# Kernel optimization log

Measured on AMD Instinct MI355X. Metric: run time of the kernel, lower is better.

Reference implementation:

```python
import jax, jax.numpy as jnp
import numpy as np

Nq, Ns, D, H, S, B, MS, MB = 30000, 400, 128, 128, 200, 256, 4, 4
P = H + 3 * D  # pred_in_feature = 512


def _lin(k, out_f, in_f):
    sc = 1.0 / np.sqrt(in_f)
    return sc * jax.random.normal(k, (out_f, in_f), jnp.float32)


def setup_inputs() -> dict:
    key = jax.random.key(0)
    ks = jax.random.split(key, 40)
    inp = {}
    inp['q_emb'] = 0.1 * jax.random.normal(ks[0], (Nq, D), jnp.float32)
    inp['s_emb'] = 0.1 * jax.random.normal(ks[1], (Ns, D), jnp.float32)
    inp['ans_emb'] = jax.random.normal(ks[2], (4, D), jnp.float32)
    inp['label_emb'] = jax.random.normal(ks[3], (2, D), jnp.float32)
    inp['gru_Wi'] = _lin(ks[4], 3 * H, 5 * D)
    inp['gru_Wh'] = _lin(ks[5], 3 * H, H)
    inp['gru_bi'] = jnp.zeros((3 * H,), jnp.float32)
    inp['gru_bh'] = jnp.zeros((3 * H,), jnp.float32)
    for i, nm in enumerate(['s2s', 's2q', 'q2q', 'q2s']):
        inp[nm + '_W'] = _lin(ks[6 + i], D, D)
        inp[nm + '_b'] = jnp.zeros((D,), jnp.float32)
    inp['l1_W'] = _lin(ks[10], P, P); inp['l1_b'] = jnp.zeros((P,), jnp.float32)
    inp['l2_W'] = _lin(ks[11], P, P); inp['l2_b'] = jnp.zeros((P,), jnp.float32)
    inp['out_W'] = _lin(ks[12], 1, P); inp['out_b'] = jnp.zeros((1,), jnp.float32)
    inp['test_mask'] = jnp.ones((S, B), jnp.float32)
    inp['valid_mask'] = jnp.ones((S, B), jnp.float32)
    inp['local_test_mask'] = jnp.ones((S, B), jnp.float32)
    inp['subject_mask'] = jnp.ones((S, B, MB), jnp.float32)
    inp['q_mask'] = jnp.ones((Nq, MS), jnp.float32)
    inp['labels'] = jnp.round(jax.random.uniform(ks[13], (S, B), jnp.float32))
    inp['ans'] = jax.random.randint(ks[14], (S, B), 0, 4, jnp.int32)
    inp['correct_ans'] = jax.random.randint(ks[15], (S, B), 0, 4, jnp.int32)
    inp['subject_ids'] = jax.random.randint(ks[16], (S, B, MB), 0, Ns, jnp.int32)
    inp['q_ids'] = jax.random.randint(ks[17], (S, B), 0, Nq, jnp.int32)
    q_map = jax.random.randint(ks[18], (Nq, MS), 0, Ns, jnp.int32)
    inp['q_map'] = q_map
    inp['edge_q'] = jnp.repeat(jnp.arange(Nq, dtype=jnp.int32), MS)  # [Nq*MS]
    inp['edge_s'] = q_map.reshape(-1)  # subject segment id per edge
    return inp


def reference(q_emb, s_emb, ans_emb, label_emb, gru_Wi, gru_Wh, gru_bi, gru_bh,
              s2s_W, s2s_b, s2q_W, s2q_b, q2q_W, q2q_b, q2s_W, q2s_b,
              l1_W, l1_b, l2_W, l2_b, out_W, out_b,
              test_mask, valid_mask, local_test_mask, subject_mask, q_mask, labels,
              ans, correct_ans, subject_ids, q_ids, q_map, edge_q, edge_s):
    n_subject = s_emb.shape[0]
    # --- GCN layer 1: question -> subject aggregation (fused segment mean) ---
    q2s_proj = q_emb @ q2s_W.T + q2s_b                      # [Nq, D]
    sums = jax.ops.segment_sum(q2s_proj[edge_q], edge_s, num_segments=n_subject)
    cnts = jax.ops.segment_sum(jnp.ones_like(edge_s, q_emb.dtype), edge_s,
                               num_segments=n_subject)       # [Ns]
    nq_s = sums / jnp.maximum(cnts, 1.0)[:, None]            # mean over neighbor questions
    sq_s = s_emb @ s2s_W.T + s2s_b
    subjects_1 = jnp.where(cnts[:, None] > 0, jnp.tanh(nq_s + sq_s), 0.0)  # [Ns, D]
    # --- GCN layer 2: subject -> question aggregation ---
    nq = jnp.sum(subjects_1[q_map] * q_mask[..., None], axis=1) / \
         jnp.sum(q_mask, axis=-1, keepdims=True)             # [Nq, D]
    questions_1 = jnp.tanh(nq @ s2q_W.T + s2q_b + q_emb @ q2q_W.T + q2q_b)
    # --- sequence features ---
    mask = (test_mask * valid_mask * local_test_mask)[..., None]  # [S,B,1]
    subjects = jnp.sum(subjects_1[subject_ids] * subject_mask[..., None], axis=2)  # [S,B,D]
    questions = questions_1[q_ids]                            # [S,B,D]
    ans_embed = ans_emb[ans] * mask
    correct_ans_embed = ans_emb[correct_ans]
    label_embed = label_emb[labels.astype(jnp.int32)] * mask
    lstm_input = jnp.concatenate(
        [ans_embed, correct_ans_embed, label_embed, questions, subjects], axis=-1)  # [S,B,5D]
    # --- GRU (PyTorch gate layout: r|z|n), dropout=0 / eval mode ---
    xp = lstm_input @ gru_Wi.T + gru_bi                      # [S,B,3H]
    hdim = gru_Wh.shape[1]
    h0 = jnp.zeros((lstm_input.shape[1], hdim), lstm_input.dtype)

    def step(h, xp_t):
        gh = h @ gru_Wh.T + gru_bh
        xr, xz, xn = jnp.split(xp_t, 3, axis=-1)
        hr, hz, hn = jnp.split(gh, 3, axis=-1)
        r = jax.nn.sigmoid(xr + hr)
        z = jax.nn.sigmoid(xz + hz)
        n = jnp.tanh(xn + r * hn)
        h_new = (1.0 - z) * n + z * h
        return h_new, h_new

    _, outs = jax.lax.scan(step, h0, xp)                     # [S,B,H]
    forward_ht = jnp.concatenate([h0[None], outs[:-1]], axis=0)  # shifted hidden states
    # --- prediction head with residual ---
    pred_input = jnp.concatenate(
        [questions, subjects, forward_ht, correct_ans_embed], axis=-1)  # [S,B,P]
    h1 = jax.nn.relu(pred_input @ l1_W.T + l1_b)
    h2 = jax.nn.relu(h1 @ l2_W.T + l2_b)
    logits = ((h2 + pred_input) @ out_W.T + out_b)[..., 0]   # [S,B]
    # BCEWithLogits: softplus(x) - x*y
    per_elem = jax.nn.softplus(logits) - logits * labels
    mask2d = mask[..., 0]
    loss = jnp.mean(per_elem * mask2d) / jnp.mean(mask2d)
    probs = jax.nn.sigmoid(logits)
    return loss, probs
```

## Files before the change

### kernel.cpp

```cpp
#include <hip/hip_runtime.h>
#include <hip/hip_bf16.h>
#include <math.h>

#define NQ 30000
#define NS 400
#define DD 128
#define HH 128
#define SS 200
#define BB 256
#define MSq 4
#define MBs 4
#define PP 512
#define SB (SS*BB)
#define G3 384
#define QPB 16
#define REPL 8
#define GBLK 32
#define TST3 (GBLK*3*1024)

typedef __hip_bfloat16 bf16;
typedef __attribute__((ext_vector_type(8))) short bf16x8;
typedef __attribute__((ext_vector_type(4))) float f32x4;
typedef __attribute__((ext_vector_type(4))) _Float16 f16x4;

__device__ __forceinline__ float sigf(float x){ return 1.0f/(1.0f+expf(-x)); }
__device__ __forceinline__ float sigf2(float x){ return 1.0f/(1.0f+__expf(-x)); }
__device__ __forceinline__ float tanhf2(float x){ return 1.0f - 2.0f/(__expf(2.0f*x)+1.0f); }
__device__ __forceinline__ float bfu2f(unsigned short u){
  unsigned int x = ((unsigned int)u)<<16;
  return __uint_as_float(x);
}

__global__ __launch_bounds__(128) void tables_k(const float* __restrict__ ans_emb,
        const float* __restrict__ label_emb, const float* __restrict__ Wi,
        float* __restrict__ Tans, float* __restrict__ Tcae, float* __restrict__ Tlab){
  int j = blockIdx.x*128 + threadIdx.x;
  if (j >= G3) return;
  const float* wr = Wi + (size_t)j*640;
  for (int a=0;a<4;a++){
    float acc=0.f;
    for (int k=0;k<DD;k++) acc += ans_emb[a*DD+k]*wr[k];
    Tans[a*G3+j]=acc;
  }
  for (int a=0;a<4;a++){
    float acc=0.f;
    for (int k=0;k<DD;k++) acc += ans_emb[a*DD+k]*wr[128+k];
    Tcae[a*G3+j]=acc;
  }
  for (int l=0;l<2;l++){
    float acc=0.f;
    for (int k=0;k<DD;k++) acc += label_emb[l*DD+k]*wr[256+k];
    Tlab[l*G3+j]=acc;
  }
}

__global__ __launch_bounds__(256) void conv_w_k(const float* __restrict__ l1W,
        const float* __restrict__ l2W, const float* __restrict__ Wi,
        bf16* __restrict__ l1Wb, bf16* __restrict__ l2Wb, bf16* __restrict__ WiB){
  int i = blockIdx.x*256 + threadIdx.x;
  if (i < 512*512){
    l1Wb[i] = __float2bfloat16(l1W[i]);
    l2Wb[i] = __float2bfloat16(l2W[i]);
  }
  if (i < 384*256){
    int j = i >> 8, k = i & 255;
    WiB[i] = __float2bfloat16(Wi[j*640 + 384 + k]);
  }
}

__global__ __launch_bounds__(128) void q2s_scatter(const float* __restrict__ q_emb,
        const float* __restrict__ W, const float* __restrict__ bias,
        const int* __restrict__ q_map, float* __restrict__ sums, float* __restrict__ cnts){
  __shared__ float qe[QPB][DD];
  int q0 = blockIdx.x*QPB;
  int tid = threadIdx.x;
  float* S = sums + (size_t)(blockIdx.x & (REPL-1))*51200;
  float* C = cnts + (size_t)(blockIdx.x & (REPL-1))*400;
  for (int r=0;r<QPB;r++) qe[r][tid] = q_emb[(size_t)(q0+r)*DD + tid];
  __syncthreads();
  float acc[QPB];
  #pragma unroll
  for (int r=0;r<QPB;r++) acc[r] = bias[tid];
  const float4* wr = (const float4*)(W + (size_t)tid*DD);
  #pragma unroll 4
  for (int k4=0;k4<DD/4;k4++){
    float4 w = wr[k4];
    #pragma unroll
    for (int r=0;r<QPB;r++){
      acc[r] += w.x*qe[r][k4*4] + w.y*qe[r][k4*4+1] + w.z*qe[r][k4*4+2] + w.w*qe[r][k4*4+3];
    }
  }
  for (int r=0;r<QPB;r++){
    int q = q0+r;
    #pragma unroll
    for (int m=0;m<MSq;m++){
      int s = q_map[q*MSq+m];
      atomicAdd(&S[(size_t)s*DD + tid], acc[r]);
      if (tid==0) atomicAdd(&C[s], 1.0f);
    }
  }
}

__global__ __launch_bounds__(128) void subjects1_k(const float* __restrict__ s_emb,
        const float* __restrict__ W, const float* __restrict__ bias,
        const float* __restrict__ sums, const float* __restrict__ cnts,
        float* __restrict__ out){
  __shared__ float se[DD];
  int s = blockIdx.x; int tid = threadIdx.x;
  se[tid] = s_emb[(size_t)s*DD+tid];
  __syncthreads();
  float acc = bias[tid];
  const float4* wr = (const float4*)(W + (size_t)tid*DD);
  for (int k4=0;k4<DD/4;k4++){
    float4 w = wr[k4];
    acc += w.x*se[k4*4] + w.y*se[k4*4+1] + w.z*se[k4*4+2] + w.w*se[k4*4+3];
  }
  float c = 0.f, sm = 0.f;
  #pragma unroll
  for (int r=0;r<REPL;r++){
    c  += cnts[r*400 + s];
    sm += sums[(size_t)r*51200 + (size_t)s*DD + tid];
  }
  float v = 0.f;
  if (c > 0.f) v = tanhf(sm/fmaxf(c,1.f) + acc);
  out[(size_t)s*DD+tid] = v;
}

__global__ __launch_bounds__(128) void questions1_k(const float* __restrict__ q_emb,
        const float* __restrict__ subj1, const int* __restrict__ q_map,
        const float* __restrict__ q_mask,
        const float* __restrict__ s2qW, const float* __restrict__ s2qb,
        const float* __restrict__ q2qW, const float* __restrict__ q2qb,
        bf16* __restrict__ q1out){
  __shared__ float qe[QPB][DD];
  __shared__ float nq[QPB][DD];
  int q0 = blockIdx.x*QPB; int tid = threadIdx.x;
  for (int r=0;r<QPB;r++){
    int q = q0+r;
    qe[r][tid] = q_emb[(size_t)q*DD+tid];
    float sum=0.f, wsum=0.f;
    #pragma unroll
    for (int m=0;m<MSq;m++){
      float w = q_mask[q*MSq+m];
      sum += subj1[(size_t)q_map[q*MSq+m]*DD + tid]*w;
      wsum += w;
    }
    nq[r][tid] = sum / wsum;
  }
  __syncthreads();
  float acc[QPB];
  #pragma unroll
  for (int r=0;r<QPB;r++) acc[r] = s2qb[tid]+q2qb[tid];
  const float4* w1 = (const float4*)(s2qW + (size_t)tid*DD);
  const float4* w2 = (const float4*)(q2qW + (size_t)tid*DD);
  #pragma unroll 2
  for (int k4=0;k4<DD/4;k4++){
    float4 a = w1[k4]; float4 b = w2[k4];
    #pragma unroll
    for (int r=0;r<QPB;r++){
      acc[r] += a.x*nq[r][k4*4] + a.y*nq[r][k4*4+1] + a.z*nq[r][k4*4+2] + a.w*nq[r][k4*4+3]
              + b.x*qe[r][k4*4] + b.y*qe[r][k4*4+1] + b.z*qe[r][k4*4+2] + b.w*qe[r][k4*4+3];
    }
  }
  for (int r=0;r<QPB;r++) q1out[(size_t)(q0+r)*DD+tid] = __float2bfloat16(tanhf(acc[r]));
}

__global__ __launch_bounds__(128) void assemble_k(const bf16* __restrict__ q1,
        const float* __restrict__ subj1, const float* __restrict__ ans_emb,
        const int* __restrict__ cans, const int* __restrict__ sub_ids,
        const float* __restrict__ sub_mask, const int* __restrict__ q_ids,
        bf16* __restrict__ pred){
  int i = blockIdx.x; int d = threadIdx.x;
  size_t base = (size_t)i*PP;
  pred[base + d] = q1[(size_t)q_ids[i]*DD + d];
  float s = 0.f;
  #pragma unroll
  for (int m=0;m<MBs;m++)
    s += subj1[(size_t)sub_ids[i*MBs+m]*DD+d]*sub_mask[i*MBs+m];
  pred[base+128+d] = __float2bfloat16(s);
  pred[base+384+d] = __float2bfloat16(ans_emb[(size_t)cans[i]*DD + d]);
}

__global__ __launch_bounds__(256) void gemm_xp(const bf16* __restrict__ pred,
        const bf16* __restrict__ WiB, const float* __restrict__ bi,
        const float* __restrict__ bh,
        const float* __restrict__ Tans, const float* __restrict__ Tcae,
        const float* __restrict__ Tlab,
        const float* __restrict__ tm, const float* __restrict__ vm,
        const float* __restrict__ lm,
        const int* __restrict__ ans, const int* __restrict__ cans,
        const float* __restrict__ labels, _Float16* __restrict__ xp3){
  int lane = threadIdx.x & 63; int wid = threadIdx.x >> 6;
  int wy = wid >> 1, wx = wid & 1;
  int mbase = blockIdx.x*128 + wy*64;
  int lr = lane & 15, kg = (lane >> 4) * 8;
  for (int ny=0; ny<3; ny++){
    int nbase = ny*128 + wx*64;
    f32x4 acc[4][4];
    #pragma unroll
    for (int i=0;i<4;i++)
      #pragma unroll
      for (int j=0;j<4;j++) acc[i][j] = (f32x4){0.f,0.f,0.f,0.f};
    for (int k=0; k<256; k+=32){
      bf16x8 af[4], bfr[4];
      #pragma unroll
      for (int mi=0;mi<4;mi++)
        af[mi] = *(const bf16x8*)(pred + (size_t)(mbase+mi*16+lr)*PP + k + kg);
      #pragma unroll
      for (int ni=0;ni<4;ni++)
        bfr[ni] = *(const bf16x8*)(WiB + (size_t)(nbase+ni*16+lr)*256 + k + kg);
      #pragma unroll
      for (int mi=0;mi<4;mi++)
        #pragma unroll
        for (int ni=0;ni<4;ni++)
          acc[mi][ni] = __builtin_amdgcn_mfma_f32_16x16x32_bf16(af[mi], bfr[ni], acc[mi][ni], 0, 0, 0);
    }
    #pragma unroll
    for (int mi=0;mi<4;mi++){
      #pragma unroll
      for (int r=0;r<4;r++){
        int row = mbase + mi*16 + (lane>>4)*4 + r;
        int t = row >> 8, b = row & 255;
        size_t base = (((size_t)t*GBLK + (b>>3))*3)*1024 + (b&7);
        float mk = tm[row]*vm[row]*lm[row];
        int a = ans[row], ca = cans[row], lb = (int)labels[row];
        #pragma unroll
        for (int ni=0;ni<4;ni++){
          int c = nbase + ni*16 + lr;
          int g = c >> 7, dd = c & 127;
          float v = acc[mi][ni][r] + bi[c]
              + mk*Tans[a*G3+c] + Tcae[ca*G3+c] + mk*Tlab[lb*G3+c];
          if (g < 2) v += bh[c];
          xp3[base + (size_t)(g*1024 + dd*8)] = (_Float16)v;
        }
      }
    }
  }
}

__global__ __launch_bounds__(512, 1) void gemm_l1l2(const bf16* __restrict__ pred,
        const bf16* __restrict__ W1, const float* __restrict__ b1,
        const bf16* __restrict__ W2, const float* __restrict__ b2,
        const float* __restrict__ outW, float* __restrict__ logits){
  __shared__ __align__(16) char hl[64*1024];
  const int lane = threadIdx.x & 63;
  const int wx = threadIdx.x >> 6;
  const int nbase = wx*64;
  const int mbase = blockIdx.x*64;
  const int lr = lane & 15, lg = lane >> 4, kg = lg*8;

  {
    f32x4 acc[4][4];
    #pragma unroll
    for (int i=0;i<4;i++)
      #pragma unroll
      for (int j=0;j<4;j++) acc[i][j] = (f32x4){0.f,0.f,0.f,0.f};
    float pres[4] = {0.f,0.f,0.f,0.f};
    for (int k=0; k<512; k+=32){
      bf16x8 af[4], bfr[4];
      #pragma unroll
      for (int mi=0;mi<4;mi++)
        af[mi] = *(const bf16x8*)(pred + (size_t)(mbase+mi*16+lr)*PP + k + kg);
      #pragma unroll
      for (int ni=0;ni<4;ni++)
        bfr[ni] = *(const bf16x8*)(W1 + (size_t)(nbase+ni*16+lr)*PP + k + kg);
      #pragma unroll
      for (int mi=0;mi<4;mi++)
        #pragma unroll
        for (int ni=0;ni<4;ni++)
          acc[mi][ni] = __builtin_amdgcn_mfma_f32_16x16x32_bf16(af[mi], bfr[ni], acc[mi][ni], 0, 0, 0);
      if (wx == 0){
        float4 o0 = *(const float4*)(outW + k + kg);
        float4 o1 = *(const float4*)(outW + k + kg + 4);
        #pragma unroll
        for (int mi=0;mi<4;mi++){
          const unsigned short* au = (const unsigned short*)&af[mi];
          pres[mi] += bfu2f(au[0])*o0.x + bfu2f(au[1])*o0.y + bfu2f(au[2])*o0.z + bfu2f(au[3])*o0.w
                    + bfu2f(au[4])*o1.x + bfu2f(au[5])*o1.y + bfu2f(au[6])*o1.z + bfu2f(au[7])*o1.w;
        }
      }
    }
    #pragma unroll
    for (int mi=0;mi<4;mi++){
      #pragma unroll
      for (int ni=0;ni<4;ni++){
        int c = nbase + ni*16 + lr;
        float bia = b1[c];
        #pragma unroll
        for (int r=0;r<4;r++){
          int rw = mi*16 + lg*4 + r;
          int addr = (rw*1024 + c*2) ^ ((rw&7)<<4);
          *(bf16*)(hl + addr) = __float2bfloat16(fmaxf(acc[mi][ni][r] + bia, 0.f));
        }
      }
    }
    if (wx == 0){
      #pragma unroll
      for (int mi=0;mi<4;mi++){
        float v = pres[mi];
        v += __shfl_xor(v, 16);
        v += __shfl_xor(v, 32);
        if (lg == 0) atomicAdd(&logits[mbase + mi*16 + lr], v);
      }
    }
  }
  __syncthreads();
  {
    f32x4 acc[4][4];
    #pragma unroll
    for (int i=0;i<4;i++)
      #pragma unroll
      for (int j=0;j<4;j++) acc[i][j] = (f32x4){0.f,0.f,0.f,0.f};
    for (int k=0; k<512; k+=32){
      bf16x8 af[4], bfr[4];
      #pragma unroll
      for (int mi=0;mi<4;mi++){
        int rw = mi*16 + lr;
        int addr = (rw*1024 + (k+kg)*2) ^ ((rw&7)<<4);
        af[mi] = *(const bf16x8*)(hl + addr);
      }
      #pragma unroll
      for (int ni=0;ni<4;ni++)
        bfr[ni] = *(const bf16x8*)(W2 + (size_t)(nbase+ni*16+lr)*PP + k + kg);
      #pragma unroll
      for (int mi=0;mi<4;mi++)
        #pragma unroll
        for (int ni=0;ni<4;ni++)
          acc[mi][ni] = __builtin_amdgcn_mfma_f32_16x16x32_bf16(af[mi], bfr[ni], acc[mi][ni], 0, 0, 0);
    }
    #pragma unroll
    for (int mi=0;mi<4;mi++){
      #pragma unroll
      for (int r=0;r<4;r++){
        int row = mbase + mi*16 + lg*4 + r;
        float p = 0.f;
        #pragma unroll
        for (int ni=0;ni<4;ni++){
          int c = nbase + ni*16 + lr;
          p += fmaxf(acc[mi][ni][r] + b2[c], 0.f) * outW[c];
        }
        p += __shfl_xor(p,1);
        p += __shfl_xor(p,2);
        p += __shfl_xor(p,4);
        p += __shfl_xor(p,8);
        if (lr == 0) atomicAdd(&logits[row], p);
      }
    }
  }
}

__global__ __launch_bounds__(512, 1) void gru_scan_mfma(const _Float16* __restrict__ xp3,
        const float* __restrict__ Wh, const float* __restrict__ bh,
        bf16* __restrict__ pred){
  __shared__ __align__(16) char hbf[8192];
  const int tid  = threadIdx.x;
  const int lane = tid & 63;
  const int w    = tid >> 6;
  const int lr   = lane & 15;
  const int lg   = lane >> 4;
  const int d    = w*16 + lr;
  const int bg0  = blockIdx.x * 8;

  union U8 { bf16x8 v; unsigned short s[8]; };
  bf16x8 wf0[4], wf1[4], wf2[4];
  #pragma unroll
  for (int kk=0; kk<4; kk++){
    #pragma unroll
    for (int g=0; g<3; g++){
      const float* src = Wh + (size_t)(g*HH + d)*HH + kk*32 + lg*8;
      U8 u;
      #pragma unroll
      for (int j=0;j<8;j++){
        bf16 bv = __float2bfloat16(src[j]);
        u.s[j] = reinterpret_cast<unsigned short&>(bv);
      }
      if (g==0) wf0[kk]=u.v; else if (g==1) wf1[kk]=u.v; else wf2[kk]=u.v;
    }
  }
  const float bh2 = bh[2*HH+d];

  int rdaddr[4];
  #pragma unroll
  for (int kk=0;kk<4;kk++) rdaddr[kk] = lr*256 + ((kk*64 + lg*16) ^ ((lr&7)<<4));
  int wraddr[4];
  #pragma unroll
  for (int q=0;q<4;q++){
    int B_ = lg*4 + q;
    wraddr[q] = B_*256 + ((2*d) ^ ((B_&7)<<4));
  }
  const int fB = tid >> 4, fblk = tid & 15;
  const int faddr = fB*256 + ((fblk*16) ^ ((fB&7)<<4));
  bf16* fptr = pred + ((size_t)bg0 + fB)*PP + 256 + fblk*8;
  const size_t PSTRIDE = (size_t)BB*PP;

  float h0=0.f, h1v=0.f, h2v=0.f, h3v=0.f;
  ((unsigned long long*)hbf)[tid]       = 0ULL;
  ((unsigned long long*)hbf)[tid + 512] = 0ULL;

  const char* xb = (const char*)(xp3 + (size_t)blockIdx.x*3*1024 + d*8 + (lg&1)*4);

#define GSET(s) \
  f16x4 x##s##r = *(const f16x4*)(xb + (size_t)(s)*TST3*2); \
  f16x4 x##s##z = *(const f16x4*)(xb + (size_t)(s)*TST3*2 + 2048); \
  f16x4 x##s##n = *(const f16x4*)(xb + (size_t)(s)*TST3*2 + 4096);
  GSET(0) GSET(1) GSET(2) GSET(3) GSET(4) GSET(5) GSET(6) GSET(7)
#undef GSET

  __syncthreads();

#define GATEQ(Q, CR, CZ, CN, HV) { \
    float r  = sigf2((float)(CR) + ac0[Q]); \
    float zg = sigf2((float)(CZ) + ac1[Q]); \
    float n  = tanhf2((float)(CN) + r*(ac2[Q] + bh2)); \
    HV = (1.f - zg)*n + zg*HV; }

#define GSTEP(s, RO_, WO_) { \
    f32x4 ac0 = (f32x4){0.f,0.f,0.f,0.f}, ac1 = ac0, ac2 = ac0; \
    _Pragma("unroll") for (int kk=0; kk<4; kk++){ \
      bf16x8 a = *(const bf16x8*)(hbf + (RO_) + rdaddr[kk]); \
      ac0 = __builtin_amdgcn_mfma_f32_16x16x32_bf16(a, wf0[kk], ac0, 0,0,0); \
      ac1 = __builtin_amdgcn_mfma_f32_16x16x32_bf16(a, wf1[kk], ac1, 0,0,0); \
      ac2 = __builtin_amdgcn_mfma_f32_16x16x32_bf16(a, wf2[kk], ac2, 0,0,0); \
    } \
    if (tid < 128){   \
      int4 hv = *(const int4*)(hbf + (RO_) + faddr); \
      *(int4*)fptr = hv; \
    } \
    fptr += PSTRIDE; \
    GATEQ(0, x##s##r.x, x##s##z.x, x##s##n.x, h0) \
    GATEQ(1, x##s##r.y, x##s##z.y, x##s##n.y, h1v) \
    GATEQ(2, x##s##r.z, x##s##z.z, x##s##n.z, h2v) \
    GATEQ(3, x##s##r.w, x##s##z.w, x##s##n.w, h3v) \
    if (lg < 2){ \
      *(bf16*)(hbf + (WO_) + wraddr[0]) = __float2bfloat16(h0); \
      *(bf16*)(hbf + (WO_) + wraddr[1]) = __float2bfloat16(h1v); \
      *(bf16*)(hbf + (WO_) + wraddr[2]) = __float2bfloat16(h2v); \
      *(bf16*)(hbf + (WO_) + wraddr[3]) = __float2bfloat16(h3v); \
    } \
    x##s##r = *(const f16x4*)(xb + (size_t)((s)+8)*TST3*2); \
    x##s##z = *(const f16x4*)(xb + (size_t)((s)+8)*TST3*2 + 2048); \
    x##s##n = *(const f16x4*)(xb + (size_t)((s)+8)*TST3*2 + 4096); \
    asm volatile("s_waitcnt lgkmcnt(0)" ::: "memory"); \
    __builtin_amdgcn_s_barrier(); \
    __builtin_amdgcn_sched_barrier(0); \
  }

  for (int it=0; it<SS/8; ++it){
    GSTEP(0, 0,    4096)
    GSTEP(1, 4096, 0)
    GSTEP(2, 0,    4096)
    GSTEP(3, 4096, 0)
    GSTEP(4, 0,    4096)
    GSTEP(5, 4096, 0)
    GSTEP(6, 0,    4096)
    GSTEP(7, 4096, 0)
    xb += (size_t)8*TST3*2;
  }
#undef GSTEP
#undef GATEQ
}

__global__ __launch_bounds__(256) void loss_probs_k(const float* __restrict__ logits,
        const float* __restrict__ labels, const float* __restrict__ tm,
        const float* __restrict__ vm, const float* __restrict__ lm,
        const float* __restrict__ out_b, float* __restrict__ out,
        float* __restrict__ lacc){
  int i = blockIdx.x*256 + threadIdx.x;
  float x = logits[i] + out_b[0];
  float lb = labels[i];
  float mk = tm[i]*vm[i]*lm[i];
  float sp = fmaxf(x,0.f) + log1pf(expf(-fabsf(x)));
  float pe = (sp - x*lb)*mk;
  out[1+i] = sigf(x);
  float v0 = pe, v1 = mk;
  for (int o=32;o>0;o>>=1){ v0 += __shfl_down(v0,o); v1 += __shfl_down(v1,o); }
  if ((threadIdx.x & 63)==0){ atomicAdd(&lacc[0], v0); atomicAdd(&lacc[1], v1); }
}

__global__ void finalize_k(const float* __restrict__ lacc, float* __restrict__ out){
  out[0] = lacc[0]/lacc[1];
}

extern "C" void kernel_launch(void* const* d_in, const int* in_sizes, int n_in,
                              void* d_out, int out_size, void* d_ws, size_t ws_size,
                              hipStream_t stream) {
  const float* q_emb   = (const float*)d_in[0];
  const float* s_emb   = (const float*)d_in[1];
  const float* ans_emb = (const float*)d_in[2];
  const float* lab_emb = (const float*)d_in[3];
  const float* gru_Wi  = (const float*)d_in[4];
  const float* gru_Wh  = (const float*)d_in[5];
  const float* gru_bi  = (const float*)d_in[6];
  const float* gru_bh  = (const float*)d_in[7];
  const float* s2s_W   = (const float*)d_in[8];
  const float* s2s_b   = (const float*)d_in[9];
  const float* s2q_W   = (const float*)d_in[10];
  const float* s2q_b   = (const float*)d_in[11];
  const float* q2q_W   = (const float*)d_in[12];
  const float* q2q_b   = (const float*)d_in[13];
  const float* q2s_W   = (const float*)d_in[14];
  const float* q2s_b   = (const float*)d_in[15];
  const float* l1_W    = (const float*)d_in[16];
  const float* l1_b    = (const float*)d_in[17];
  const float* l2_W    = (const float*)d_in[18];
  const float* l2_b    = (const float*)d_in[19];
  const float* out_W   = (const float*)d_in[20];
  const float* out_b   = (const float*)d_in[21];
  const float* tm      = (const float*)d_in[22];
  const float* vm      = (const float*)d_in[23];
  const float* lm      = (const float*)d_in[24];
  const float* smask   = (const float*)d_in[25];
  const float* q_mask  = (const float*)d_in[26];
  const float* labels  = (const float*)d_in[27];
  const int*   ans     = (const int*)d_in[28];
  const int*   cans    = (const int*)d_in[29];
  const int*   sub_ids = (const int*)d_in[30];
  const int*   q_ids   = (const int*)d_in[31];
  const int*   q_map   = (const int*)d_in[32];

  char* wsb = (char*)d_ws;
  size_t off = 0;
  auto alloc = [&](size_t bytes) -> char* {
    char* p = wsb + off;
    off += (bytes + 255) & ~(size_t)255;
    return p;
  };
  float* sums   = (float*)alloc((size_t)REPL*51200*4);
  float* cnts   = (float*)alloc((size_t)REPL*400*4);
  float* subj1  = (float*)alloc(51200*4);
  float* Tans   = (float*)alloc(4*G3*4);
  float* Tcae   = (float*)alloc(4*G3*4);
  float* Tlab   = (float*)alloc(2*G3*4);
  float* lacc   = (float*)alloc(2*4);
  float* logits = (float*)alloc((size_t)SB*4);
  bf16*  l1Wb   = (bf16*) alloc((size_t)512*512*2);
  bf16*  l2Wb   = (bf16*) alloc((size_t)512*512*2);
  bf16*  WiB    = (bf16*) alloc((size_t)384*256*2);
  bf16*  q1     = (bf16*) alloc((size_t)NQ*DD*2);
  bf16*  pred   = (bf16*) alloc((size_t)SB*PP*2);
  _Float16* xp3 = (_Float16*)alloc(((size_t)SS+8)*TST3*2);
  float* out    = (float*)d_out;

  hipMemsetAsync(sums, 0, (size_t)REPL*(51200+400)*sizeof(float), stream);
  hipMemsetAsync(lacc, 0, 2*sizeof(float), stream);
  hipMemsetAsync(logits, 0, (size_t)SB*sizeof(float), stream);

  tables_k<<<dim3(3), dim3(128), 0, stream>>>(ans_emb, lab_emb, gru_Wi, Tans, Tcae, Tlab);
  conv_w_k<<<dim3(1024), dim3(256), 0, stream>>>(l1_W, l2_W, gru_Wi, l1Wb, l2Wb, WiB);
  q2s_scatter<<<dim3(NQ/QPB), dim3(128), 0, stream>>>(q_emb, q2s_W, q2s_b, q_map, sums, cnts);
  subjects1_k<<<dim3(NS), dim3(128), 0, stream>>>(s_emb, s2s_W, s2s_b, sums, cnts, subj1);
  questions1_k<<<dim3(NQ/QPB), dim3(128), 0, stream>>>(q_emb, subj1, q_map, q_mask,
                                                       s2q_W, s2q_b, q2q_W, q2q_b, q1);
  assemble_k<<<dim3(SB), dim3(128), 0, stream>>>(q1, subj1, ans_emb, cans, sub_ids, smask, q_ids, pred);
  gemm_xp<<<dim3(400), dim3(256), 0, stream>>>(pred, WiB, gru_bi, gru_bh, Tans, Tcae, Tlab,
                                               tm, vm, lm, ans, cans, labels, xp3);
  gru_scan_mfma<<<dim3(GBLK), dim3(512), 0, stream>>>(xp3, gru_Wh, gru_bh, pred);
  gemm_l1l2<<<dim3(SB/64), dim3(512), 0, stream>>>(pred, l1Wb, l1_b, l2Wb, l2_b, out_W, logits);
  loss_probs_k<<<dim3(SB/256), dim3(256), 0, stream>>>(logits, labels, tm, vm, lm, out_b, out, lacc);
  finalize_k<<<dim3(1), dim3(1), 0, stream>>>(lacc, out);
}
```

Measured before the change: 922.8 us.

## Retune scatter replication, grid-stride assemble, split xp GEMM grid, shallower GRU prefetch

```diff
diff --git a/kernel.cpp b/kernel.cpp
--- a/kernel.cpp
+++ b/kernel.cpp
@@ -14,7 +14,7 @@
 #define SB (SS*BB)
 #define G3 384
 #define QPB 16
-#define REPL 8
+#define REPL 64
 #define GBLK 32
 #define TST3 (GBLK*3*1024)
 
@@ -24,8 +24,12 @@
 typedef __attribute__((ext_vector_type(4))) _Float16 f16x4;
 
 __device__ __forceinline__ float sigf(float x){ return 1.0f/(1.0f+expf(-x)); }
-__device__ __forceinline__ float sigf2(float x){ return 1.0f/(1.0f+__expf(-x)); }
-__device__ __forceinline__ float tanhf2(float x){ return 1.0f - 2.0f/(__expf(2.0f*x)+1.0f); }
+__device__ __forceinline__ float sigr(float x){
+  return __builtin_amdgcn_rcpf(1.0f + __expf(-x));
+}
+__device__ __forceinline__ float tanhr(float x){
+  return 1.0f - 2.0f*__builtin_amdgcn_rcpf(__expf(2.0f*x) + 1.0f);
+}
 __device__ __forceinline__ float bfu2f(unsigned short u){
   unsigned int x = ((unsigned int)u)<<16;
   return __uint_as_float(x);
@@ -116,7 +120,6 @@
     acc += w.x*se[k4*4] + w.y*se[k4*4+1] + w.z*se[k4*4+2] + w.w*se[k4*4+3];
   }
   float c = 0.f, sm = 0.f;
-  #pragma unroll
   for (int r=0;r<REPL;r++){
     c  += cnts[r*400 + s];
     sm += sums[(size_t)r*51200 + (size_t)s*DD + tid];
@@ -165,20 +168,23 @@
   for (int r=0;r<QPB;r++) q1out[(size_t)(q0+r)*DD+tid] = __float2bfloat16(tanhf(acc[r]));
 }
 
-__global__ __launch_bounds__(128) void assemble_k(const bf16* __restrict__ q1,
+__global__ __launch_bounds__(256) void assemble_k(const bf16* __restrict__ q1,
         const float* __restrict__ subj1, const float* __restrict__ ans_emb,
         const int* __restrict__ cans, const int* __restrict__ sub_ids,
         const float* __restrict__ sub_mask, const int* __restrict__ q_ids,
         bf16* __restrict__ pred){
-  int i = blockIdx.x; int d = threadIdx.x;
-  size_t base = (size_t)i*PP;
-  pred[base + d] = q1[(size_t)q_ids[i]*DD + d];
-  float s = 0.f;
-  #pragma unroll
-  for (int m=0;m<MBs;m++)
-    s += subj1[(size_t)sub_ids[i*MBs+m]*DD+d]*sub_mask[i*MBs+m];
-  pred[base+128+d] = __float2bfloat16(s);
-  pred[base+384+d] = __float2bfloat16(ans_emb[(size_t)cans[i]*DD + d]);
+  const int total = SB*DD;
+  for (int idx = blockIdx.x*256 + threadIdx.x; idx < total; idx += 1024*256){
+    int i = idx >> 7, d = idx & 127;
+    size_t base = (size_t)i*PP;
+    pred[base + d] = q1[(size_t)q_ids[i]*DD + d];
+    float s = 0.f;
+    #pragma unroll
+    for (int m=0;m<MBs;m++)
+      s += subj1[(size_t)sub_ids[i*MBs+m]*DD+d]*sub_mask[i*MBs+m];
+    pred[base+128+d] = __float2bfloat16(s);
+    pred[base+384+d] = __float2bfloat16(ans_emb[(size_t)cans[i]*DD + d]);
+  }
 }
 
 __global__ __launch_bounds__(256) void gemm_xp(const bf16* __restrict__ pred,
@@ -193,46 +199,44 @@
   int lane = threadIdx.x & 63; int wid = threadIdx.x >> 6;
   int wy = wid >> 1, wx = wid & 1;
   int mbase = blockIdx.x*128 + wy*64;
+  int nbase = blockIdx.y*128 + wx*64;
   int lr = lane & 15, kg = (lane >> 4) * 8;
-  for (int ny=0; ny<3; ny++){
-    int nbase = ny*128 + wx*64;
-    f32x4 acc[4][4];
-    #pragma unroll
-    for (int i=0;i<4;i++)
-      #pragma unroll
-      for (int j=0;j<4;j++) acc[i][j] = (f32x4){0.f,0.f,0.f,0.f};
-    for (int k=0; k<256; k+=32){
-      bf16x8 af[4], bfr[4];
-      #pragma unroll
-      for (int mi=0;mi<4;mi++)
-        af[mi] = *(const bf16x8*)(pred + (size_t)(mbase+mi*16+lr)*PP + k + kg);
+  f32x4 acc[4][4];
+  #pragma unroll
+  for (int i=0;i<4;i++)
+    #pragma unroll
+    for (int j=0;j<4;j++) acc[i][j] = (f32x4){0.f,0.f,0.f,0.f};
+  for (int k=0; k<256; k+=32){
+    bf16x8 af[4], bfr[4];
+    #pragma unroll
+    for (int mi=0;mi<4;mi++)
+      af[mi] = *(const bf16x8*)(pred + (size_t)(mbase+mi*16+lr)*PP + k + kg);
+    #pragma unroll
+    for (int ni=0;ni<4;ni++)
+      bfr[ni] = *(const bf16x8*)(WiB + (size_t)(nbase+ni*16+lr)*256 + k + kg);
+    #pragma unroll
+    for (int mi=0;mi<4;mi++)
       #pragma unroll
       for (int ni=0;ni<4;ni++)
-        bfr[ni] = *(const bf16x8*)(WiB + (size_t)(nbase+ni*16+lr)*256 + k + kg);
-      #pragma unroll
-      for (int mi=0;mi<4;mi++)
-        #pragma unroll
-        for (int ni=0;ni<4;ni++)
-          acc[mi][ni] = __builtin_amdgcn_mfma_f32_16x16x32_bf16(af[mi], bfr[ni], acc[mi][ni], 0, 0, 0);
-    }
-    #pragma unroll
-    for (int mi=0;mi<4;mi++){
-      #pragma unroll
-      for (int r=0;r<4;r++){
-        int row = mbase + mi*16 + (lane>>4)*4 + r;
-        int t = row >> 8, b = row & 255;
-        size_t base = (((size_t)t*GBLK + (b>>3))*3)*1024 + (b&7);
-        float mk = tm[row]*vm[row]*lm[row];
-        int a = ans[row], ca = cans[row], lb = (int)labels[row];
-        #pragma unroll
-        for (int ni=0;ni<4;ni++){
-          int c = nbase + ni*16 + lr;
-          int g = c >> 7, dd = c & 127;
-          float v = acc[mi][ni][r] + bi[c]
-              + mk*Tans[a*G3+c] + Tcae[ca*G3+c] + mk*Tlab[lb*G3+c];
-          if (g < 2) v += bh[c];
-          xp3[base + (size_t)(g*1024 + dd*8)] = (_Float16)v;
-        }
+        acc[mi][ni] = __builtin_amdgcn_mfma_f32_16x16x32_bf16(af[mi], bfr[ni], acc[mi][ni], 0, 0, 0);
+  }
+  #pragma unroll
+  for (int mi=0;mi<4;mi++){
+    #pragma unroll
+    for (int r=0;r<4;r++){
+      int row = mbase + mi*16 + (lane>>4)*4 + r;
+      int t = row >> 8, b = row & 255;
+      size_t base = (((size_t)t*GBLK + (b>>3))*3)*1024 + (b&7);
+      float mk = tm[row]*vm[row]*lm[row];
+      int a = ans[row], ca = cans[row], lb = (int)labels[row];
+      #pragma unroll
+      for (int ni=0;ni<4;ni++){
+        int c = nbase + ni*16 + lr;
+        int g = c >> 7, dd = c & 127;
+        float v = acc[mi][ni][r] + bi[c]
+            + mk*Tans[a*G3+c] + Tcae[ca*G3+c] + mk*Tlab[lb*G3+c];
+        if (g < 2) v += bh[c];
+        xp3[base + (size_t)(g*1024 + dd*8)] = (_Float16)v;
       }
     }
   }
@@ -248,7 +252,6 @@
   const int nbase = wx*64;
   const int mbase = blockIdx.x*64;
   const int lr = lane & 15, lg = lane >> 4, kg = lg*8;
-
   {
     f32x4 acc[4][4];
     #pragma unroll
@@ -398,23 +401,23 @@
   ((unsigned long long*)hbf)[tid + 512] = 0ULL;
 
   const char* xb = (const char*)(xp3 + (size_t)blockIdx.x*3*1024 + d*8 + (lg&1)*4);
-
-#define GSET(s) \
-  f16x4 x##s##r = *(const f16x4*)(xb + (size_t)(s)*TST3*2); \
-  f16x4 x##s##z = *(const f16x4*)(xb + (size_t)(s)*TST3*2 + 2048); \
-  f16x4 x##s##n = *(const f16x4*)(xb + (size_t)(s)*TST3*2 + 4096);
-  GSET(0) GSET(1) GSET(2) GSET(3) GSET(4) GSET(5) GSET(6) GSET(7)
-#undef GSET
+  f16x4 xrA = *(const f16x4*)(xb);
+  f16x4 xzA = *(const f16x4*)(xb + 2048);
+  f16x4 xnA = *(const f16x4*)(xb + 4096);
+  f16x4 xrB = *(const f16x4*)(xb + (size_t)TST3*2);
+  f16x4 xzB = *(const f16x4*)(xb + (size_t)TST3*2 + 2048);
+  f16x4 xnB = *(const f16x4*)(xb + (size_t)TST3*2 + 4096);
+  const char* xt = xb + 2*(size_t)TST3*2;
 
   __syncthreads();
 
 #define GATEQ(Q, CR, CZ, CN, HV) { \
-    float r  = sigf2((float)(CR) + ac0[Q]); \
-    float zg = sigf2((float)(CZ) + ac1[Q]); \
-    float n  = tanhf2((float)(CN) + r*(ac2[Q] + bh2)); \
+    float r  = sigr((float)(CR) + ac0[Q]); \
+    float zg = sigr((float)(CZ) + ac1[Q]); \
+    float n  = tanhr((float)(CN) + r*(ac2[Q] + bh2)); \
     HV = (1.f - zg)*n + zg*HV; }
 
-#define GSTEP(s, RO_, WO_) { \
+#define GSTEP(RO_, WO_, XR, XZ, XN) { \
     f32x4 ac0 = (f32x4){0.f,0.f,0.f,0.f}, ac1 = ac0, ac2 = ac0; \
     _Pragma("unroll") for (int kk=0; kk<4; kk++){ \
       bf16x8 a = *(const bf16x8*)(hbf + (RO_) + rdaddr[kk]); \
@@ -422,39 +425,33 @@
       ac1 = __builtin_amdgcn_mfma_f32_16x16x32_bf16(a, wf1[kk], ac1, 0,0,0); \
       ac2 = __builtin_amdgcn_mfma_f32_16x16x32_bf16(a, wf2[kk], ac2, 0,0,0); \
     } \
-    if (tid < 128){   \
+    if (tid < 128){ \
       int4 hv = *(const int4*)(hbf + (RO_) + faddr); \
       *(int4*)fptr = hv; \
     } \
     fptr += PSTRIDE; \
-    GATEQ(0, x##s##r.x, x##s##z.x, x##s##n.x, h0) \
-    GATEQ(1, x##s##r.y, x##s##z.y, x##s##n.y, h1v) \
-    GATEQ(2, x##s##r.z, x##s##z.z, x##s##n.z, h2v) \
-    GATEQ(3, x##s##r.w, x##s##z.w, x##s##n.w, h3v) \
+    GATEQ(0, (XR).x, (XZ).x, (XN).x, h0) \
+    GATEQ(1, (XR).y, (XZ).y, (XN).y, h1v) \
+    GATEQ(2, (XR).z, (XZ).z, (XN).z, h2v) \
+    GATEQ(3, (XR).w, (XZ).w, (XN).w, h3v) \
     if (lg < 2){ \
       *(bf16*)(hbf + (WO_) + wraddr[0]) = __float2bfloat16(h0); \
       *(bf16*)(hbf + (WO_) + wraddr[1]) = __float2bfloat16(h1v); \
       *(bf16*)(hbf + (WO_) + wraddr[2]) = __float2bfloat16(h2v); \
       *(bf16*)(hbf + (WO_) + wraddr[3]) = __float2bfloat16(h3v); \
     } \
-    x##s##r = *(const f16x4*)(xb + (size_t)((s)+8)*TST3*2); \
-    x##s##z = *(const f16x4*)(xb + (size_t)((s)+8)*TST3*2 + 2048); \
-    x##s##n = *(const f16x4*)(xb + (size_t)((s)+8)*TST3*2 + 4096); \
+    XR = *(const f16x4*)(xt); \
+    XZ = *(const f16x4*)(xt + 2048); \
+    XN = *(const f16x4*)(xt + 4096); \
+    xt += (size_t)TST3*2; \
     asm volatile("s_waitcnt lgkmcnt(0)" ::: "memory"); \
     __builtin_amdgcn_s_barrier(); \
     __builtin_amdgcn_sched_barrier(0); \
   }
 
-  for (int it=0; it<SS/8; ++it){
-    GSTEP(0, 0,    4096)
-    GSTEP(1, 4096, 0)
-    GSTEP(2, 0,    4096)
-    GSTEP(3, 4096, 0)
-    GSTEP(4, 0,    4096)
-    GSTEP(5, 4096, 0)
-    GSTEP(6, 0,    4096)
-    GSTEP(7, 4096, 0)
-    xb += (size_t)8*TST3*2;
+  for (int t=0; t<SS; t+=2){
+    GSTEP(0,    4096, xrA, xzA, xnA)
+    GSTEP(4096, 0,    xrB, xzB, xnB)
   }
 #undef GSTEP
 #undef GATEQ
@@ -538,7 +535,7 @@
   bf16*  WiB    = (bf16*) alloc((size_t)384*256*2);
   bf16*  q1     = (bf16*) alloc((size_t)NQ*DD*2);
   bf16*  pred   = (bf16*) alloc((size_t)SB*PP*2);
-  _Float16* xp3 = (_Float16*)alloc(((size_t)SS+8)*TST3*2);
+  _Float16* xp3 = (_Float16*)alloc(((size_t)SS+4)*TST3*2);
   float* out    = (float*)d_out;
 
   hipMemsetAsync(sums, 0, (size_t)REPL*(51200+400)*sizeof(float), stream);
@@ -551,9 +548,9 @@
   subjects1_k<<<dim3(NS), dim3(128), 0, stream>>>(s_emb, s2s_W, s2s_b, sums, cnts, subj1);
   questions1_k<<<dim3(NQ/QPB), dim3(128), 0, stream>>>(q_emb, subj1, q_map, q_mask,
                                                        s2q_W, s2q_b, q2q_W, q2q_b, q1);
-  assemble_k<<<dim3(SB), dim3(128), 0, stream>>>(q1, subj1, ans_emb, cans, sub_ids, smask, q_ids, pred);
-  gemm_xp<<<dim3(400), dim3(256), 0, stream>>>(pred, WiB, gru_bi, gru_bh, Tans, Tcae, Tlab,
-                                               tm, vm, lm, ans, cans, labels, xp3);
+  assemble_k<<<dim3(1024), dim3(256), 0, stream>>>(q1, subj1, ans_emb, cans, sub_ids, smask, q_ids, pred);
+  gemm_xp<<<dim3(400,3), dim3(256), 0, stream>>>(pred, WiB, gru_bi, gru_bh, Tans, Tcae, Tlab,
+                                                 tm, vm, lm, ans, cans, labels, xp3);
   gru_scan_mfma<<<dim3(GBLK), dim3(512), 0, stream>>>(xp3, gru_Wh, gru_bh, pred);
   gemm_l1l2<<<dim3(SB/64), dim3(512), 0, stream>>>(pred, l1Wb, l1_b, l2Wb, l2_b, out_W, logits);
   loss_probs_k<<<dim3(SB/256), dim3(256), 0, stream>>>(logits, labels, tm, vm, lm, out_b, out, lacc);
```

Measured after the change: 779.8 us. 1.18x faster.
